# Optimization experiments

Hardware: AMD Instinct MI355X
Metric: run time of the kernel (lower is better)

## Reference

```python
import jax, jax.numpy as jnp
import numpy as np

B, S, D_MODEL, D_HEAD = 8, 2048, 1024, 128
MAX_ROUNDS = 3
THRESH = 0.1
SCALE = 1.0 / np.sqrt(float(D_HEAD))


def setup_inputs() -> dict:
    key = jax.random.key(0)
    ks = jax.random.split(key, 12)

    def lin(k, out_d, in_d):
        # torch Linear weight layout [out, in], y = x @ W.T + b
        return (jax.random.normal(k, (out_d, in_d), jnp.float32) / np.sqrt(float(in_d))).astype(jnp.float32)

    thesis_w = lin(ks[3], D_HEAD, D_HEAD)
    return {
        "x": jax.random.normal(ks[0], (B, S, D_MODEL), jnp.float32),
        "wq": lin(ks[1], D_HEAD, D_MODEL),
        "wk": lin(ks[2], D_HEAD, D_MODEL),
        "wv": lin(ks[4], D_HEAD, D_MODEL),
        "thesis_w": thesis_w,  # antithesis weight is -thesis_w per __init__
        "thesis_b": 0.02 * jax.random.normal(ks[5], (D_HEAD,), jnp.float32),
        "anti_b": 0.02 * jax.random.normal(ks[6], (D_HEAD,), jnp.float32),
        "s_w1": lin(ks[7], D_HEAD, 3 * D_HEAD),
        "s_b1": jnp.zeros((D_HEAD,), jnp.float32),
        "s_w2": lin(ks[8], D_HEAD, D_HEAD),
        "s_b2": jnp.zeros((D_HEAD,), jnp.float32),
        "g_w": lin(ks[9], 1, 2 * D_HEAD),
        "g_b": jnp.zeros((1,), jnp.float32),
    }


def reference(x, wq, wk, wv, thesis_w, thesis_b, anti_b, s_w1, s_b1, s_w2, s_b2, g_w, g_b):
    # q/k/v projections (no bias)
    q = jnp.einsum("bsm,hm->bsh", x, wq)
    k = jnp.einsum("bsm,hm->bsh", x, wk)
    v = jnp.einsum("bsm,hm->bsh", x, wv)

    attn = jax.nn.softmax(jnp.einsum("bqh,bkh->bqk", q, k) * SCALE, axis=-1)
    # dropout is identity at eval time
    cur = jnp.einsum("bqk,bkh->bqh", attn, v)  # [B,S,Dh]

    # attn_weights and v never change across rounds, so thesis/antithesis are
    # round-invariant: compute the context projections once.
    context = cur
    thesis = context @ thesis_w.T + thesis_b
    anti = context @ (-thesis_w).T + anti_b  # antithesis weight = -thesis weight

    active = jnp.ones((B, S), dtype=bool)
    for _ in range(MAX_ROUNDS):
        # emulate `if not active_mask.any(): break` under jit
        any_active = jnp.any(active)
        am = active[..., None].astype(x.dtype)
        at, aa, ac = thesis * am, anti * am, cur * am

        h = jax.nn.relu(jnp.concatenate([at, aa, ac], axis=-1) @ s_w1.T + s_b1)
        synth = h @ s_w2.T + s_b2
        gate = jax.nn.sigmoid(jnp.concatenate([ac, synth], axis=-1) @ g_w.T + g_b)
        update = gate * (synth - ac) * 0.1
        new = cur + update  # applied to ALL tokens, matching original

        stable = jnp.linalg.norm(update, axis=-1) < THRESH  # new - cur == update
        cur = jnp.where(any_active, new, cur)
        active = jnp.where(any_active, active & ~stable, active)
    return cur
```

## Files before the change

kernel.cpp:

```cpp
#include <hip/hip_runtime.h>
#include <hip/hip_bf16.h>

#define B_   8
#define S_   2048
#define DM   1024
#define DH   128
#define BS_  16384
#define SCALE_  0.08838834764831845f
#define SCALE2_ 0.12751744f

typedef unsigned short u16;
typedef unsigned int   u32;
typedef _Float16 half8 __attribute__((ext_vector_type(8)));
typedef __bf16   bf16x8 __attribute__((ext_vector_type(8)));
typedef float    f32x4 __attribute__((ext_vector_type(4)));
typedef u32      u32x4 __attribute__((ext_vector_type(4)));

union H8 { u32x4 v; u32 u[4]; half8 h; bf16x8 b; };

__device__ __forceinline__ float bf2f(u16 u) {
    union { u32 i; float f; } w; w.i = ((u32)u) << 16; return w.f;
}
__device__ __forceinline__ void unpack8(uint4 v, float* f) {
    f[0] = bf2f(v.x & 0xffff); f[1] = bf2f(v.x >> 16);
    f[2] = bf2f(v.y & 0xffff); f[3] = bf2f(v.y >> 16);
    f[4] = bf2f(v.z & 0xffff); f[5] = bf2f(v.z >> 16);
    f[6] = bf2f(v.w & 0xffff); f[7] = bf2f(v.w >> 16);
}
__device__ __forceinline__ float ldE(const void* b, size_t i, int isbf16) {
    return isbf16 ? bf2f(((const u16*)b)[i]) : ((const float*)b)[i];
}
__device__ __forceinline__ void ld8(const void* b, size_t i, int isbf16, float* f) {
    if (isbf16) {
        unpack8(*(const uint4*)((const u16*)b + i), f);
    } else {
        float4 a = *(const float4*)((const float*)b + i);
        float4 c = *(const float4*)((const float*)b + i + 4);
        f[0] = a.x; f[1] = a.y; f[2] = a.z; f[3] = a.w;
        f[4] = c.x; f[5] = c.y; f[6] = c.z; f[7] = c.w;
    }
}
__device__ __forceinline__ u32 f2pk(float v) {
    _Float16 h = (_Float16)v;
    _Float16 l = (_Float16)(v - (float)h);
    union { _Float16 f; u16 u; } a, b; a.f = h; b.f = l;
    return ((u32)a.u << 16) | (u32)b.u;
}
__device__ __forceinline__ void split8(const float* f, u32x4& hi, u32x4& lo) {
    u32 H[8], L[8];
#pragma unroll
    for (int j = 0; j < 8; ++j) {
        _Float16 h = (_Float16)f[j];
        _Float16 l = (_Float16)(f[j] - (float)h);
        union { _Float16 x; u16 u; } a, b; a.x = h; b.x = l;
        H[j] = a.u; L[j] = b.u;
    }
    hi = (u32x4){H[0] | (H[1] << 16), H[2] | (H[3] << 16), H[4] | (H[5] << 16), H[6] | (H[7] << 16)};
    lo = (u32x4){L[0] | (L[1] << 16), L[2] | (L[3] << 16), L[4] | (L[5] << 16), L[6] | (L[7] << 16)};
}
__device__ __forceinline__ u32 permHI(u32 eB, u32 eA) { return __builtin_amdgcn_perm(eB, eA, 0x07060302u); }
__device__ __forceinline__ u16 f2h(float v) { union { _Float16 f; u16 u; } a; a.f = (_Float16)v; return a.u; }
__device__ __forceinline__ float h2f(u16 u) { union { _Float16 f; u16 u; } a; a.u = u; return (float)a.f; }

__global__ void init_kernel(const void* x, int* flag, int* active, int* counts) {
    int i = blockIdx.x * 256 + threadIdx.x;
    if (i < BS_) active[i] = 1;
    if (i < 4) counts[i] = (i == 0) ? BS_ : 0;
    if (i == 0) {
        const u16* w = (const u16*)x;
        int sane = 0;
        for (int t = 0; t < 256; ++t) {
            int e = (w[2 * t] >> 7) & 0xFF;
            if (e >= 100 && e <= 135) ++sane;
        }
        *flag = (sane >= 192) ? 1 : 0;
    }
}

__global__ __launch_bounds__(256) void prepack_w_kernel(
    const void* __restrict__ wq, const void* __restrict__ wk, const void* __restrict__ wv,
    const int* __restrict__ flag, u32x4* __restrict__ wpk)
{
    const int isb = *flag;
    const int gid = blockIdx.x * 256 + threadIdx.x;
    const int l  = gid & 63;
    const int t  = (gid >> 6) & 7;
    const int ks = (gid >> 9) & 31;
    const int z  = gid >> 14;
    const void* W = (z == 0) ? wq : (z == 1) ? wk : wv;
    const int row = 16 * t + (l & 15);
    const int k0  = ks * 32 + 8 * (l >> 4);
    const size_t base = ((((size_t)z * 32 + ks) * 16) + 2 * t) * 64 + l;
    if (isb) {
        uint4 v = *(const uint4*)((const u16*)W + (size_t)row * DM + k0);
        wpk[base] = (u32x4){v.x, v.y, v.z, v.w};
    } else {
        float f[8];
        ld8(W, (size_t)row * DM + k0, 0, f);
        u32x4 hi, lo;
        split8(f, hi, lo);
        wpk[base]      = hi;
        wpk[base + 64] = lo;
    }
}

__global__ __launch_bounds__(256) void qkv_kernel(
    const void* __restrict__ x, const u32x4* __restrict__ wpk,
    const int* __restrict__ flag, u32* __restrict__ qout,
    u32x4* __restrict__ kfrag, u32x4* __restrict__ vfrag)
{
    const int isb = *flag;
    const int z = blockIdx.z;
    const int bx = blockIdx.x;
    const int m0 = ((bx & 7) * 32 + (bx >> 3)) * 64;
    const int tid = threadIdx.x;
    const int wave = tid >> 6, lane = tid & 63;
    const int qd = lane >> 4, c = lane & 15;

    __shared__ u32x4 WLraw[2][16][64];
    u32x4 (*WLb)[2][8][64] = (u32x4(*)[2][8][64])WLraw;
    u32x4 (*WLf)[8][2][64] = (u32x4(*)[8][2][64])WLraw;
    u16 (*TS)[136] = (u16(*)[136])WLraw;

    const u32x4* wz = wpk + (size_t)z * (32 * 16 * 64);
    const size_t arow = (size_t)(m0 + wave * 16 + c) * DM + 8 * qd;

#define STAGE2(i_, b_)                                                            \
    {                                                                             \
        _Pragma("unroll")                                                         \
        for (int _j = 0; _j < 4; ++_j) {                                          \
            const int _g = wave * 4 + _j, _ksub = _g >> 3, _t = _g & 7;           \
            __builtin_amdgcn_global_load_lds(                                     \
                (const __attribute__((address_space(1))) u32*)(                   \
                    wz + ((size_t)(2 * (i_) + _ksub) * 16 + 2 * _t) * 64 + lane), \
                (__attribute__((address_space(3))) u32*)&WLb[b_][_ksub][_t][0],   \
                16, 0, 0);                                                        \
        }                                                                         \
    }
#define STAGE_W(ks_, b_)                                                          \
    {                                                                             \
        const u32x4* _src = wz + ((size_t)(ks_) * 16 + 4 * wave) * 64 + lane;     \
        _Pragma("unroll")                                                         \
        for (int _j = 0; _j < 4; ++_j) {                                          \
            __builtin_amdgcn_global_load_lds(                                     \
                (const __attribute__((address_space(1))) u32*)(_src + _j * 64),   \
                (__attribute__((address_space(3))) u32*)&WLf[b_][2 * wave + (_j >> 1)][_j & 1][0], \
                16, 0, 0);                                                        \
        }                                                                         \
    }

    f32x4 acc[8] = {};

    if (isb) {
        const u16* xb = (const u16*)x;
        uint4 A0 = *(const uint4*)(xb + arow);
        uint4 A1 = *(const uint4*)(xb + arow + 32);
        STAGE2(0, 0);
        uint4 A0n = *(const uint4*)(xb + arow + 64);
        uint4 A1n = *(const uint4*)(xb + arow + 96);
        __syncthreads();
        for (int i = 0; i < 16; ++i) {
            const int cb = i & 1;
            if (i + 1 < 16) STAGE2(i + 1, cb ^ 1);
            H8 Ah0; Ah0.v = (u32x4){A0.x, A0.y, A0.z, A0.w};
            H8 Ah1; Ah1.v = (u32x4){A1.x, A1.y, A1.z, A1.w};
#pragma unroll
            for (int t = 0; t < 8; ++t) {
                H8 bh; bh.v = WLb[cb][0][t][lane];
                acc[t] = __builtin_amdgcn_mfma_f32_16x16x32_bf16(Ah0.b, bh.b, acc[t], 0, 0, 0);
            }
#pragma unroll
            for (int t = 0; t < 8; ++t) {
                H8 bh; bh.v = WLb[cb][1][t][lane];
                acc[t] = __builtin_amdgcn_mfma_f32_16x16x32_bf16(Ah1.b, bh.b, acc[t], 0, 0, 0);
            }
            A0 = A0n; A1 = A1n;
            if (i + 2 < 16) {
                A0n = *(const uint4*)(xb + arow + (size_t)(i + 2) * 64);
                A1n = *(const uint4*)(xb + arow + (size_t)(i + 2) * 64 + 32);
            }
            __syncthreads();
        }
    } else {
        float Ar[8], Arn[8];
        ld8(x, arow, 0, Ar);
        STAGE_W(0, 0);
        ld8(x, arow + 32, 0, Arn);
        __syncthreads();
        for (int ks = 0; ks < 32; ++ks) {
            const int cb = ks & 1;
            if (ks + 1 < 32) STAGE_W(ks + 1, cb ^ 1);
            H8 Ah, Al;
            split8(Ar, Ah.v, Al.v);
#pragma unroll
            for (int t = 0; t < 8; ++t) {
                H8 bh, bl;
                bh.v = WLf[cb][t][0][lane]; bl.v = WLf[cb][t][1][lane];
                acc[t] = __builtin_amdgcn_mfma_f32_16x16x32_f16(Al.h, bh.h, acc[t], 0, 0, 0);
                acc[t] = __builtin_amdgcn_mfma_f32_16x16x32_f16(Ah.h, bl.h, acc[t], 0, 0, 0);
                acc[t] = __builtin_amdgcn_mfma_f32_16x16x32_f16(Ah.h, bh.h, acc[t], 0, 0, 0);
            }
#pragma unroll
            for (int j = 0; j < 8; ++j) Ar[j] = Arn[j];
            if (ks + 2 < 32) ld8(x, arow + (size_t)(ks + 2) * 32, 0, Arn);
            __syncthreads();
        }
    }
#undef STAGE2
#undef STAGE_W

    if (z == 0) {
#pragma unroll
        for (int r = 0; r < 4; ++r) {
            const int row = m0 + wave * 16 + qd * 4 + r;
            u32* op = qout + (size_t)row * DH + c;
#pragma unroll
            for (int t = 0; t < 8; ++t) op[t * 16] = f2pk(acc[t][r]);
        }
    } else {
#pragma unroll
        for (int t = 0; t < 8; ++t)
#pragma unroll
            for (int r = 0; r < 4; ++r)
                TS[wave * 16 + qd * 4 + r][16 * t + c] = f2h(acc[t][r]);
        __syncthreads();
        if (z == 1) {
#pragma unroll
            for (int i = 0; i < 4; ++i) {
                const int f = tid + 256 * i;
                const int lf = f & 63, ks = (f >> 6) & 3, sub = f >> 8;
                const int key = sub * 16 + (lf & 15);
                const int d0  = ks * 32 + 8 * (lf >> 4);
                u32 w[4];
#pragma unroll
                for (int q = 0; q < 4; ++q)
                    w[q] = (u32)TS[key][d0 + 2 * q] | ((u32)TS[key][d0 + 2 * q + 1] << 16);
                kfrag[((size_t)(m0 / 16 + sub) * 4 + ks) * 64 + lf] = (u32x4){w[0], w[1], w[2], w[3]};
            }
        } else {
#pragma unroll
            for (int i = 0; i < 4; ++i) {
                const int f = tid + 256 * i;
                const int lf = f & 63, t = (f >> 6) & 7, sub = f >> 9;
                const int kb2 = sub * 32 + 8 * (lf >> 4);
                const int dh  = 16 * t + (lf & 15);
                u32 w[4];
#pragma unroll
                for (int q = 0; q < 4; ++q)
                    w[q] = (u32)TS[kb2 + 2 * q][dh] | ((u32)TS[kb2 + 2 * q + 1][dh] << 16);
                vfrag[((size_t)(m0 / 32 + sub) * 8 + t) * 64 + lf] = (u32x4){w[0], w[1], w[2], w[3]};
            }
        }
    }
}

template <bool WRITE_PARTIAL>
__device__ __forceinline__ void attn_body(
    const u32* qp, const u32x4* __restrict__ kfrag, const u32x4* __restrict__ vfrag,
    u16* outO, u16* outL, float* cur,
    int b, int q0, int kt0, int kt1, int part)
{
    const int tid = threadIdx.x;
    const int wave = tid >> 6, lane = tid & 63;
    const int qd = lane >> 4, c = lane & 15;

    __shared__ __align__(16) u16 PB[4][640];

    H8 Qh[4];
    {
        const u32* qr = qp + ((size_t)b * S_ + q0 + wave * 16 + c) * DH;
#pragma unroll
        for (int ks = 0; ks < 4; ++ks) {
            uint4 e0 = *(const uint4*)(qr + ks * 32 + qd * 8);
            uint4 e1 = *(const uint4*)(qr + ks * 32 + qd * 8 + 4);
            Qh[ks].u[0] = permHI(e0.y, e0.x); Qh[ks].u[1] = permHI(e0.w, e0.z);
            Qh[ks].u[2] = permHI(e1.y, e1.x); Qh[ks].u[3] = permHI(e1.w, e1.z);
        }
    }

    f32x4 O[8] = {};
    float lsum[4] = {};

    const u32x4* kb0 = kfrag + (size_t)b * 128 * 256;
    const u32x4* vb0 = vfrag + (size_t)b * 64 * 512;

    for (int kt = kt0; kt < kt1; ++kt) {
        const u32x4* kf = kb0 + (size_t)kt * 512;
        const u32x4* vf = vb0 + (size_t)kt * 512;

        f32x4 S0 = {}, S1 = {};
        __builtin_amdgcn_s_setprio(1);
#pragma unroll
        for (int ks = 0; ks < 4; ++ks) {
            H8 kh;
            kh.v = kf[ks * 64 + lane];
            S0 = __builtin_amdgcn_mfma_f32_16x16x32_f16(Qh[ks].h, kh.h, S0, 0, 0, 0);
            kh.v = kf[256 + ks * 64 + lane];
            S1 = __builtin_amdgcn_mfma_f32_16x16x32_f16(Qh[ks].h, kh.h, S1, 0, 0, 0);
        }
        __builtin_amdgcn_s_setprio(0);

        u16* pw = PB[wave];
#pragma unroll
        for (int r = 0; r < 4; ++r) {
            float e0 = exp2f(fmaf(S0[r], SCALE2_, -4.0f));
            float e1 = exp2f(fmaf(S1[r], SCALE2_, -4.0f));
            lsum[r] += e0 + e1;
            pw[(4 * qd + r) * 40 + c]      = f2h(e0);
            pw[(4 * qd + r) * 40 + 16 + c] = f2h(e1);
        }

        uint4 ev = *(const uint4*)&pw[c * 40 + 8 * qd];
        H8 Ph;
        Ph.u[0] = ev.x; Ph.u[1] = ev.y; Ph.u[2] = ev.z; Ph.u[3] = ev.w;

        __builtin_amdgcn_s_setprio(1);
#pragma unroll
        for (int t = 0; t < 8; ++t) {
            H8 vh;
            vh.v = vf[t * 64 + lane];
            O[t] = __builtin_amdgcn_mfma_f32_16x16x32_f16(Ph.h, vh.h, O[t], 0, 0, 0);
        }
        __builtin_amdgcn_s_setprio(0);
    }

    if (WRITE_PARTIAL) {
        float lred[4];
#pragma unroll
        for (int r = 0; r < 4; ++r) {
            float l = lsum[r];
            l += __shfl_xor(l, 1); l += __shfl_xor(l, 2);
            l += __shfl_xor(l, 4); l += __shfl_xor(l, 8);
            lred[r] = l;
        }
        const size_t rb = (size_t)b * S_ + q0 + wave * 16 + 4 * qd;
        u16* Op = outO + (size_t)part * ((size_t)BS_ * DH);
#pragma unroll
        for (int t = 0; t < 8; ++t)
#pragma unroll
            for (int r = 0; r < 4; ++r)
                Op[(rb + r) * DH + t * 16 + c] = f2h(O[t][r]);
        if (c == 0) {
            u16* lp = outL + (size_t)part * BS_;
#pragma unroll
            for (int r = 0; r < 4; ++r) lp[rb + r] = f2h(lred[r]);
        }
    } else {
        float linv[4];
#pragma unroll
        for (int r = 0; r < 4; ++r) {
            float l = lsum[r];
            l += __shfl_xor(l, 1); l += __shfl_xor(l, 2);
            l += __shfl_xor(l, 4); l += __shfl_xor(l, 8);
            linv[r] = 1.0f / l;
        }
        const size_t rb = (size_t)b * S_ + q0 + wave * 16 + 4 * qd;
#pragma unroll
        for (int t = 0; t < 8; ++t)
#pragma unroll
            for (int r = 0; r < 4; ++r)
                cur[(rb + r) * DH + t * 16 + c] = O[t][r] * linv[r];
    }
}

__global__ __launch_bounds__(256) void attn_kernel(
    const u32* qp, const u32x4* __restrict__ kfrag, const u32x4* __restrict__ vfrag, float* cur)
{
    const int rid = blockIdx.x + 32 * blockIdx.y;
    attn_body<false>(qp, kfrag, vfrag, nullptr, nullptr, cur,
                     rid & 7, ((rid >> 3) & 31) * 64, 0, S_ / 32, 0);
}

__global__ __launch_bounds__(256) void attn_split_kernel(
    const u32* qp, const u32x4* __restrict__ kfrag, const u32x4* __restrict__ vfrag,
    u16* __restrict__ Opart, u16* __restrict__ lpart)
{
    const int rid = blockIdx.x + 32 * (blockIdx.y + 8 * blockIdx.z);
    const int b    = rid & 7;
    const int qx   = (rid >> 3) & 31;
    const int part = rid >> 8;
    const int quart = S_ / 128;
    attn_body<true>(qp, kfrag, vfrag, Opart, lpart, nullptr,
                    b, qx * 64, part * quart, (part + 1) * quart, part);
}

__global__ __launch_bounds__(256) void combine_kernel(
    const u16* __restrict__ Opart, const u16* __restrict__ lpart,
    float* __restrict__ cur)
{
    const size_t N1 = (size_t)BS_ * DH;
    const size_t i0 = ((size_t)blockIdx.x * 256 + threadIdx.x) * 16;
    const int row = (int)(i0 >> 7);
    const float lt = h2f(lpart[row]) + h2f(lpart[BS_ + row])
                   + h2f(lpart[2 * BS_ + row]) + h2f(lpart[3 * BS_ + row]);
    const float linv = 1.0f / lt;
    float acc[16] = {};
#pragma unroll
    for (int p = 0; p < 4; ++p) {
        const u16* op = Opart + (size_t)p * N1 + i0;
        uint4 v0 = *(const uint4*)op;
        uint4 v1 = *(const uint4*)(op + 8);
        const u32 w[8] = {v0.x, v0.y, v0.z, v0.w, v1.x, v1.y, v1.z, v1.w};
#pragma unroll
        for (int j = 0; j < 8; ++j) {
            acc[2 * j]     += h2f((u16)(w[j] & 0xffff));
            acc[2 * j + 1] += h2f((u16)(w[j] >> 16));
        }
    }
#pragma unroll
    for (int t = 0; t < 4; ++t)
        *(float4*)(cur + i0 + t * 4) = make_float4(
            acc[4*t] * linv, acc[4*t+1] * linv, acc[4*t+2] * linv, acc[4*t+3] * linv);
}

__global__ __launch_bounds__(256) void prepack_rw_kernel(
    const void* __restrict__ tw, const void* __restrict__ w1, const void* __restrict__ w2,
    const int* __restrict__ flag, u32x4* __restrict__ pk)
{
    const int isb = *flag;
    const int gid = blockIdx.x * 256 + threadIdx.x;
    const int l = gid & 63, t = (gid >> 6) & 7, ks = (gid >> 9) & 3, mat = gid >> 11;
    const int row = 16 * t + (l & 15);
    const int k0  = ks * 32 + 8 * (l >> 4);
    float f[8];
    if (mat == 0)      ld8(tw, (size_t)row * DH + k0, isb, f);
    else if (mat <= 3) ld8(w1, (size_t)row * 384 + (mat - 1) * 128 + k0, isb, f);
    else               ld8(w2, (size_t)row * DH + k0, isb, f);
    u32x4 hi, lo;
    split8(f, hi, lo);
    const size_t base = (((size_t)mat * 4 + ks) * 16 + 2 * t) * 64 + l;
    pk[base] = hi; pk[base + 64] = lo;
}

struct Afrag { H8 h[4], l[4]; };
__device__ __forceinline__ void splitA(const float (&A)[4][8], Afrag& F) {
#pragma unroll
    for (int ks = 0; ks < 4; ++ks) split8(A[ks], F.h[ks].v, F.l[ks].v);
}

__global__ __launch_bounds__(256) void round_kernel(
    const float* cur0, const float* curr,
    const u32x4* __restrict__ pk, u16* __restrict__ T0,
    const void* __restrict__ tb, const void* __restrict__ ab,
    const void* __restrict__ b1, const void* __restrict__ b2,
    const void* __restrict__ gw, const void* __restrict__ gb,
    const int* __restrict__ flag, int* active, int* counts, int r,
    float* cur_out, void* dout)
{
    const int isb = *flag;
    const int tok0 = blockIdx.x * 32;
    const int tid = threadIdx.x;
    const bool last = (dout != nullptr);

    if (counts[r] <= 0) {
        if (last) {
            for (int e = tid; e < 32 * DH; e += 256) {
                size_t idx = (size_t)tok0 * DH + e;
                float v = curr[idx];
                if (isb) ((__hip_bfloat16*)dout)[idx] = __float2bfloat16(v);
                else     ((float*)dout)[idx] = v;
            }
        }
        return;
    }

    const int wave = tid >> 6, lane = tid & 63;
    const int qd = lane >> 4, c = lane & 15;
    const int rowg = wave >> 1, colh = wave & 1;

    __shared__ u32x4 WB[2][4][8][64];
    __shared__ u16 TS[32][132];
    __shared__ float actS[32], tbS[128], abS[128], b1S[128], b2S[128], gwS[256];
    __shared__ int blkcnt;

    auto stageB = [&](int mat, int buf) {
#pragma unroll
        for (int j = 0; j < 8; ++j) {
            const int g = wave * 8 + j, ks = g >> 3, t = g & 7;
            __builtin_amdgcn_global_load_lds(
                (const __attribute__((address_space(1))) u32*)(
                    pk + (((size_t)mat * 4 + ks) * 16 + 2 * t) * 64 + lane),
                (__attribute__((address_space(3))) u32*)&WB[buf][ks][t][0],
                16, 0, 0);
        }
    };
    auto stageF = [&](int mat, int h, int buf) {
#pragma unroll
        for (int j = 0; j < 8; ++j) {
            const int g = wave * 8 + j, kl = g >> 4, p = (g >> 3) & 1, t = g & 7;
            __builtin_amdgcn_global_load_lds(
                (const __attribute__((address_space(1))) u32*)(
                    pk + (((size_t)mat * 4 + 2 * h + kl) * 16 + 2 * t + p) * 64 + lane),
                (__attribute__((address_space(3))) u32*)&WB[buf][kl * 2 + p][t][0],
                16, 0, 0);
        }
    };
    auto gemmB = [&](const Afrag& F, int buf, f32x4 (&acc)[4]) {
#pragma unroll
        for (int ks = 0; ks < 4; ++ks)
#pragma unroll
            for (int tl = 0; tl < 4; ++tl) {
                H8 bh; bh.v = WB[buf][ks][4 * colh + tl][lane];
                acc[tl] = __builtin_amdgcn_mfma_f32_16x16x32_f16(F.l[ks].h, bh.h, acc[tl], 0, 0, 0);
                acc[tl] = __builtin_amdgcn_mfma_f32_16x16x32_f16(F.h[ks].h, bh.h, acc[tl], 0, 0, 0);
            }
    };
    auto gemmFh = [&](const Afrag& F, int h, int buf, f32x4 (&acc)[4]) {
#pragma unroll
        for (int kl = 0; kl < 2; ++kl) {
            const int ks = 2 * h + kl;
#pragma unroll
            for (int tl = 0; tl < 4; ++tl) {
                H8 bh, bl;
                bh.v = WB[buf][kl * 2][4 * colh + tl][lane];
                bl.v = WB[buf][kl * 2 + 1][4 * colh + tl][lane];
                acc[tl] = __builtin_amdgcn_mfma_f32_16x16x32_f16(F.l[ks].h, bh.h, acc[tl], 0, 0, 0);
                acc[tl] = __builtin_amdgcn_mfma_f32_16x16x32_f16(F.h[ks].h, bl.h, acc[tl], 0, 0, 0);
                acc[tl] = __builtin_amdgcn_mfma_f32_16x16x32_f16(F.h[ks].h, bh.h, acc[tl], 0, 0, 0);
            }
        }
    };
    auto STAGE = [&](int mat, int buf) { if (isb) stageB(mat, buf); else stageF(mat, 0, buf); };
    auto GEMM = [&](int mat, const Afrag& F, int buf, f32x4 (&acc)[4]) {
        if (isb) {
            gemmB(F, buf, acc);
        } else {
            gemmFh(F, 0, buf, acc);
            __syncthreads();
            stageF(mat, 1, buf);
            __syncthreads();
            gemmFh(F, 1, buf, acc);
        }
    };

    if (r == 0) STAGE(0, 0); else STAGE(1, 1);
    if (tid < 32) actS[tid] = active[tok0 + tid] ? 1.0f : 0.0f;
    if (tid < 128) {
        tbS[tid] = ldE(tb, tid, isb); abS[tid] = ldE(ab, tid, isb);
        b1S[tid] = ldE(b1, tid, isb); b2S[tid] = ldE(b2, tid, isb);
    }
    gwS[tid] = ldE(gw, tid, isb);
    if (tid == 0) blkcnt = 0;
    const float gbf = ldE(gb, 0, isb);

    const int rowl = 16 * rowg + c;
    const int hr   = 16 * rowg + 4 * qd;

    Afrag FA;
    if (r == 0) {
        float A1[4][8];
        const float* cr = cur0 + (size_t)(tok0 + rowl) * DH;
#pragma unroll
        for (int ks = 0; ks < 4; ++ks) {
            *(float4*)&A1[ks][0] = *(const float4*)(cr + ks * 32 + 8 * qd);
            *(float4*)&A1[ks][4] = *(const float4*)(cr + ks * 32 + 8 * qd + 4);
        }
        splitA(A1, FA);
    } else {
        for (int i = tid; i < 32 * 64; i += 256) {
            const int row = i >> 6, c2 = (i & 63) * 2;
            *(u32*)&TS[row][c2] = *(const u32*)&T0[(size_t)(tok0 + row) * DH + c2];
        }
    }
    __syncthreads();

    if (r == 0) {
        STAGE(1, 1);
        f32x4 accT[4] = {};
        GEMM(0, FA, 0, accT);
#pragma unroll
        for (int tl = 0; tl < 4; ++tl)
#pragma unroll
            for (int rr = 0; rr < 4; ++rr)
                TS[hr + rr][16 * (4 * colh + tl) + c] = f2h(accT[tl][rr]);
        __syncthreads();
        for (int i = tid; i < 32 * 64; i += 256) {
            const int row = i >> 6, c2 = (i & 63) * 2;
            *(u32*)&T0[(size_t)(tok0 + row) * DH + c2] = *(const u32*)&TS[row][c2];
        }
    }

    STAGE(2, 0);
    f32x4 acc1[4] = {};
    const float am_r = actS[rowl];
    {
        float Ac[4][8];
#pragma unroll
        for (int ks = 0; ks < 4; ++ks)
#pragma unroll
            for (int j = 0; j < 8; ++j) {
                const int k = ks * 32 + 8 * qd + j;
                Ac[ks][j] = (h2f(TS[rowl][k]) + tbS[k]) * am_r;
            }
        Afrag FC; splitA(Ac, FC);
        GEMM(1, FC, 1, acc1);
    }
    __syncthreads();

    STAGE(3, 1);
    {
        float Ac[4][8];
#pragma unroll
        for (int ks = 0; ks < 4; ++ks)
#pragma unroll
            for (int j = 0; j < 8; ++j) {
                const int k = ks * 32 + 8 * qd + j;
                Ac[ks][j] = (abS[k] - h2f(TS[rowl][k])) * am_r;
            }
        Afrag FC; splitA(Ac, FC);
        GEMM(2, FC, 0, acc1);
    }
    __syncthreads();

    STAGE(4, 0);
    {
        float Ac[4][8];
        const float* cr = curr + (size_t)(tok0 + rowl) * DH;
#pragma unroll
        for (int ks = 0; ks < 4; ++ks) {
            float4 a0 = *(const float4*)(cr + ks * 32 + 8 * qd);
            float4 a1 = *(const float4*)(cr + ks * 32 + 8 * qd + 4);
            Ac[ks][0] = a0.x * am_r; Ac[ks][1] = a0.y * am_r;
            Ac[ks][2] = a0.z * am_r; Ac[ks][3] = a0.w * am_r;
            Ac[ks][4] = a1.x * am_r; Ac[ks][5] = a1.y * am_r;
            Ac[ks][6] = a1.z * am_r; Ac[ks][7] = a1.w * am_r;
        }
        Afrag FC; splitA(Ac, FC);
        GEMM(3, FC, 1, acc1);
    }
#pragma unroll
    for (int tl = 0; tl < 4; ++tl)
#pragma unroll
        for (int rr = 0; rr < 4; ++rr) {
            const int col = 16 * (4 * colh + tl) + c;
            TS[hr + rr][col] = f2h(fmaxf(acc1[tl][rr] + b1S[col], 0.0f));
        }
    __syncthreads();

    {
        float Ac[4][8];
#pragma unroll
        for (int ks = 0; ks < 4; ++ks)
#pragma unroll
            for (int j = 0; j < 8; ++j)
                Ac[ks][j] = h2f(TS[rowl][ks * 32 + 8 * qd + j]);
        Afrag FC; splitA(Ac, FC);
        f32x4 acc2[4] = {};
        GEMM(4, FC, 0, acc2);
        __syncthreads();
#pragma unroll
        for (int tl = 0; tl < 4; ++tl)
#pragma unroll
            for (int rr = 0; rr < 4; ++rr) {
                const int col = 16 * (4 * colh + tl) + c;
                TS[hr + rr][col] = f2h(acc2[tl][rr] + b2S[col]);
            }
    }
    __syncthreads();

    const int tok = tid >> 3, d0 = (tid & 7) * 16;
    const float am = actS[tok];
    const float* cp = curr + (size_t)(tok0 + tok) * DH + d0;
    float cv[16];
#pragma unroll
    for (int t = 0; t < 4; ++t) {
        float4 vv = *(const float4*)(cp + t * 4);
        cv[t * 4] = vv.x; cv[t * 4 + 1] = vv.y; cv[t * 4 + 2] = vv.z; cv[t * 4 + 3] = vv.w;
    }
    float srow[16];
#pragma unroll
    for (int e = 0; e < 16; ++e) srow[e] = h2f(TS[tok][d0 + e]);
    float gp = 0.0f;
#pragma unroll
    for (int e = 0; e < 16; ++e)
        gp += cv[e] * am * gwS[d0 + e] + srow[e] * gwS[128 + d0 + e];
    gp += __shfl_xor(gp, 1, 8);
    gp += __shfl_xor(gp, 2, 8);
    gp += __shfl_xor(gp, 4, 8);
    const float gate = 1.0f / (1.0f + __expf(-(gp + gbf)));
    float ss = 0.0f; float up[16];
#pragma unroll
    for (int e = 0; e < 16; ++e) {
        float u = gate * (srow[e] - cv[e] * am) * 0.1f;
        up[e] = u; ss += u * u;
    }
    ss += __shfl_xor(ss, 1, 8);
    ss += __shfl_xor(ss, 2, 8);
    ss += __shfl_xor(ss, 4, 8);
    const bool stable = sqrtf(ss) < 0.1f;

    if (last) {
        size_t off = (size_t)(tok0 + tok) * DH + d0;
        if (isb) {
            __hip_bfloat16* op = (__hip_bfloat16*)dout + off;
#pragma unroll
            for (int e = 0; e < 16; ++e) op[e] = __float2bfloat16(cv[e] + up[e]);
        } else {
            float* op = (float*)dout + off;
#pragma unroll
            for (int t = 0; t < 4; ++t)
                *(float4*)(op + t * 4) = make_float4(cv[t * 4] + up[t * 4], cv[t * 4 + 1] + up[t * 4 + 1],
                                                     cv[t * 4 + 2] + up[t * 4 + 2], cv[t * 4 + 3] + up[t * 4 + 3]);
        }
    } else {
        float* op = cur_out + (size_t)(tok0 + tok) * DH + d0;
#pragma unroll
        for (int t = 0; t < 4; ++t)
            *(float4*)(op + t * 4) = make_float4(cv[t * 4] + up[t * 4], cv[t * 4 + 1] + up[t * 4 + 1],
                                                 cv[t * 4 + 2] + up[t * 4 + 2], cv[t * 4 + 3] + up[t * 4 + 3]);
    }
    const int newact = (am > 0.0f && !stable) ? 1 : 0;
    if ((tid & 7) == 0) {
        active[tok0 + tok] = newact;
        if (newact) atomicAdd(&blkcnt, 1);
    }
    __syncthreads();
    if (tid == 0 && blkcnt > 0) atomicAdd(&counts[r + 1], blkcnt);
}

extern "C" void kernel_launch(void* const* d_in, const int* in_sizes, int n_in,
                              void* d_out, int out_size, void* d_ws, size_t ws_size,
                              hipStream_t stream) {
    const void* x  = d_in[0];
    const void* wq = d_in[1];
    const void* wk = d_in[2];
    const void* wv = d_in[3];
    const void* tw = d_in[4];
    const void* tb = d_in[5];
    const void* ab = d_in[6];
    const void* w1 = d_in[7];
    const void* b1 = d_in[8];
    const void* w2 = d_in[9];
    const void* b2 = d_in[10];
    const void* gw = d_in[11];
    const void* gb = d_in[12];

    u32* ws = (u32*)d_ws;
    const size_t N1 = (size_t)BS_ * DH;
    u32* qp = ws;
    u32* kp = ws + N1;
    u32* vp = ws + 2 * N1;
    int* active = (int*)(ws + 3 * N1);
    int* counts = active + BS_;
    int* flag   = counts + 4;
    float* cur0  = (float*)qp;
    float* cur_r = (float*)kp;
    u16* Opart16 = (u16*)(ws + 3 * N1 + 32768);
    u16* lpart16 = (u16*)(ws + 5 * N1 + 32768);
    const bool big_ws = ws_size >= (size_t)42300000;
    u32x4* wpk = (u32x4*)(ws + 3 * N1 + 32768);
    u32x4* pkRW = (u32x4*)vp;
    u16*   T0c  = (u16*)(vp + 131072);
    u32x4* kfragP = (u32x4*)kp;
    u32x4* vfragP = (u32x4*)vp;

    init_kernel<<<dim3(BS_ / 256), 256, 0, stream>>>(x, flag, active, counts);
    prepack_w_kernel<<<dim3(192), 256, 0, stream>>>(wq, wk, wv, flag, wpk);
    qkv_kernel<<<dim3(BS_ / 64, 1, 3), 256, 0, stream>>>(x, wpk, flag, qp, kfragP, vfragP);
    if (big_ws) {
        attn_split_kernel<<<dim3(S_ / 64, B_, 4), 256, 0, stream>>>(qp, kfragP, vfragP, Opart16, lpart16);
        combine_kernel<<<dim3(512), 256, 0, stream>>>(Opart16, lpart16, cur0);
    } else {
        attn_kernel<<<dim3(S_ / 64, B_), 256, 0, stream>>>(qp, kfragP, vfragP, cur0);
    }
    prepack_rw_kernel<<<dim3(40), 256, 0, stream>>>(tw, w1, w2, flag, pkRW);
    round_kernel<<<dim3(BS_ / 32), 256, 0, stream>>>(
        cur0, cur0, pkRW, T0c, tb, ab, b1, b2, gw, gb, flag, active, counts, 0, cur_r, nullptr);
    round_kernel<<<dim3(BS_ / 32), 256, 0, stream>>>(
        cur0, cur_r, pkRW, T0c, tb, ab, b1, b2, gw, gb, flag, active, counts, 1, cur_r, nullptr);
    round_kernel<<<dim3(BS_ / 32), 256, 0, stream>>>(
        cur0, cur_r, pkRW, T0c, tb, ab, b1, b2, gw, gb, flag, active, counts, 2, cur_r, d_out);
}
```

Baseline: 254.7 us.

## Halve round-kernel token tile to 16 and stream weights in half-K stages

The round kernel now handles 16 tokens per block instead of 32, doubling the grid to 1024 blocks. Each wave owns two output column tiles across all 16 rows. Weight staging is split into half-K (bf16) or quarter-K (fp32) chunks in a smaller double-buffered LDS area, which lets the next chunk load while the current one is multiplied. This is meant to raise parallelism and occupancy for the small per-round GEMMs, at the cost of loading each weight matrix twice as often per token and adding more barriers.

```diff
diff --git a/kernel.cpp b/kernel.cpp
--- a/kernel.cpp
+++ b/kernel.cpp
@@ -448,13 +448,13 @@
     float* cur_out, void* dout)
 {
     const int isb = *flag;
-    const int tok0 = blockIdx.x * 32;
+    const int tok0 = blockIdx.x * 16;
     const int tid = threadIdx.x;
     const bool last = (dout != nullptr);
 
     if (counts[r] <= 0) {
         if (last) {
-            for (int e = tid; e < 32 * DH; e += 256) {
+            for (int e = tid; e < 16 * DH; e += 256) {
                 size_t idx = (size_t)tok0 * DH + e;
                 float v = curr[idx];
                 if (isb) ((__hip_bfloat16*)dout)[idx] = __float2bfloat16(v);
@@ -466,124 +466,80 @@
 
     const int wave = tid >> 6, lane = tid & 63;
     const int qd = lane >> 4, c = lane & 15;
-    const int rowg = wave >> 1, colh = wave & 1;
-
-    __shared__ u32x4 WB[2][4][8][64];
-    __shared__ u16 TS[32][132];
-    __shared__ float actS[32], tbS[128], abS[128], b1S[128], b2S[128], gwS[256];
+
+    __shared__ u32x4 WB[2][2][8][64];
+    __shared__ u16 TS[16][132];
+    __shared__ float actS[16], tbS[128], abS[128], b1S[128], b2S[128], gwS[256];
     __shared__ int blkcnt;
 
-    auto stageB = [&](int mat, int buf) {
-#pragma unroll
-        for (int j = 0; j < 8; ++j) {
-            const int g = wave * 8 + j, ks = g >> 3, t = g & 7;
+    auto stageBh = [&](int mat, int h) {
+#pragma unroll
+        for (int j = 0; j < 4; ++j) {
+            const int g = wave * 4 + j, kl = g >> 3, t = g & 7;
             __builtin_amdgcn_global_load_lds(
                 (const __attribute__((address_space(1))) u32*)(
-                    pk + (((size_t)mat * 4 + ks) * 16 + 2 * t) * 64 + lane),
-                (__attribute__((address_space(3))) u32*)&WB[buf][ks][t][0],
+                    pk + (((size_t)mat * 4 + 2 * h + kl) * 16 + 2 * t) * 64 + lane),
+                (__attribute__((address_space(3))) u32*)&WB[h][kl][t][0],
                 16, 0, 0);
         }
     };
-    auto stageF = [&](int mat, int h, int buf) {
-#pragma unroll
-        for (int j = 0; j < 8; ++j) {
-            const int g = wave * 8 + j, kl = g >> 4, p = (g >> 3) & 1, t = g & 7;
+    auto gemmBh = [&](const Afrag& F, int h, f32x4 (&acc)[2]) {
+#pragma unroll
+        for (int kl = 0; kl < 2; ++kl) {
+            const int ks = 2 * h + kl;
+#pragma unroll
+            for (int tl = 0; tl < 2; ++tl) {
+                H8 bh; bh.v = WB[h][kl][2 * wave + tl][lane];
+                acc[tl] = __builtin_amdgcn_mfma_f32_16x16x32_f16(F.l[ks].h, bh.h, acc[tl], 0, 0, 0);
+                acc[tl] = __builtin_amdgcn_mfma_f32_16x16x32_f16(F.h[ks].h, bh.h, acc[tl], 0, 0, 0);
+            }
+        }
+    };
+    auto stageFq = [&](int mat, int q, int buf) {
+#pragma unroll
+        for (int j = 0; j < 4; ++j) {
+            const int g = wave * 4 + j, p = g & 1, t = g >> 1;
             __builtin_amdgcn_global_load_lds(
                 (const __attribute__((address_space(1))) u32*)(
-                    pk + (((size_t)mat * 4 + 2 * h + kl) * 16 + 2 * t + p) * 64 + lane),
-                (__attribute__((address_space(3))) u32*)&WB[buf][kl * 2 + p][t][0],
+                    pk + (((size_t)mat * 4 + q) * 16 + 2 * t + p) * 64 + lane),
+                (__attribute__((address_space(3))) u32*)&WB[buf][p][t][0],
                 16, 0, 0);
         }
     };
-    auto gemmB = [&](const Afrag& F, int buf, f32x4 (&acc)[4]) {
-#pragma unroll
-        for (int ks = 0; ks < 4; ++ks)
-#pragma unroll
-            for (int tl = 0; tl < 4; ++tl) {
-                H8 bh; bh.v = WB[buf][ks][4 * colh + tl][lane];
-                acc[tl] = __builtin_amdgcn_mfma_f32_16x16x32_f16(F.l[ks].h, bh.h, acc[tl], 0, 0, 0);
-                acc[tl] = __builtin_amdgcn_mfma_f32_16x16x32_f16(F.h[ks].h, bh.h, acc[tl], 0, 0, 0);
-            }
-    };
-    auto gemmFh = [&](const Afrag& F, int h, int buf, f32x4 (&acc)[4]) {
-#pragma unroll
-        for (int kl = 0; kl < 2; ++kl) {
-            const int ks = 2 * h + kl;
-#pragma unroll
-            for (int tl = 0; tl < 4; ++tl) {
-                H8 bh, bl;
-                bh.v = WB[buf][kl * 2][4 * colh + tl][lane];
-                bl.v = WB[buf][kl * 2 + 1][4 * colh + tl][lane];
-                acc[tl] = __builtin_amdgcn_mfma_f32_16x16x32_f16(F.l[ks].h, bh.h, acc[tl], 0, 0, 0);
-                acc[tl] = __builtin_amdgcn_mfma_f32_16x16x32_f16(F.h[ks].h, bl.h, acc[tl], 0, 0, 0);
-                acc[tl] = __builtin_amdgcn_mfma_f32_16x16x32_f16(F.h[ks].h, bh.h, acc[tl], 0, 0, 0);
-            }
-        }
-    };
-    auto STAGE = [&](int mat, int buf) { if (isb) stageB(mat, buf); else stageF(mat, 0, buf); };
-    auto GEMM = [&](int mat, const Afrag& F, int buf, f32x4 (&acc)[4]) {
-        if (isb) {
-            gemmB(F, buf, acc);
-        } else {
-            gemmFh(F, 0, buf, acc);
-            __syncthreads();
-            stageF(mat, 1, buf);
-            __syncthreads();
-            gemmFh(F, 1, buf, acc);
-        }
-    };
-
-    if (r == 0) STAGE(0, 0); else STAGE(1, 1);
-    if (tid < 32) actS[tid] = active[tok0 + tid] ? 1.0f : 0.0f;
-    if (tid < 128) {
-        tbS[tid] = ldE(tb, tid, isb); abS[tid] = ldE(ab, tid, isb);
-        b1S[tid] = ldE(b1, tid, isb); b2S[tid] = ldE(b2, tid, isb);
-    }
-    gwS[tid] = ldE(gw, tid, isb);
-    if (tid == 0) blkcnt = 0;
-    const float gbf = ldE(gb, 0, isb);
-
-    const int rowl = 16 * rowg + c;
-    const int hr   = 16 * rowg + 4 * qd;
-
-    Afrag FA;
-    if (r == 0) {
-        float A1[4][8];
-        const float* cr = cur0 + (size_t)(tok0 + rowl) * DH;
-#pragma unroll
-        for (int ks = 0; ks < 4; ++ks) {
-            *(float4*)&A1[ks][0] = *(const float4*)(cr + ks * 32 + 8 * qd);
-            *(float4*)&A1[ks][4] = *(const float4*)(cr + ks * 32 + 8 * qd + 4);
-        }
-        splitA(A1, FA);
-    } else {
-        for (int i = tid; i < 32 * 64; i += 256) {
-            const int row = i >> 6, c2 = (i & 63) * 2;
-            *(u32*)&TS[row][c2] = *(const u32*)&T0[(size_t)(tok0 + row) * DH + c2];
-        }
-    }
-    __syncthreads();
-
-    if (r == 0) {
-        STAGE(1, 1);
-        f32x4 accT[4] = {};
-        GEMM(0, FA, 0, accT);
-#pragma unroll
-        for (int tl = 0; tl < 4; ++tl)
-#pragma unroll
-            for (int rr = 0; rr < 4; ++rr)
-                TS[hr + rr][16 * (4 * colh + tl) + c] = f2h(accT[tl][rr]);
-        __syncthreads();
-        for (int i = tid; i < 32 * 64; i += 256) {
-            const int row = i >> 6, c2 = (i & 63) * 2;
-            *(u32*)&T0[(size_t)(tok0 + row) * DH + c2] = *(const u32*)&TS[row][c2];
-        }
-    }
-
-    STAGE(2, 0);
-    f32x4 acc1[4] = {};
-    const float am_r = actS[rowl];
-    {
+    auto gemmFq = [&](const Afrag& F, int q, int buf, f32x4 (&acc)[2]) {
+#pragma unroll
+        for (int tl = 0; tl < 2; ++tl) {
+            H8 bh, bl;
+            bh.v = WB[buf][0][2 * wave + tl][lane];
+            bl.v = WB[buf][1][2 * wave + tl][lane];
+            acc[tl] = __builtin_amdgcn_mfma_f32_16x16x32_f16(F.l[q].h, bh.h, acc[tl], 0, 0, 0);
+            acc[tl] = __builtin_amdgcn_mfma_f32_16x16x32_f16(F.h[q].h, bl.h, acc[tl], 0, 0, 0);
+            acc[tl] = __builtin_amdgcn_mfma_f32_16x16x32_f16(F.h[q].h, bh.h, acc[tl], 0, 0, 0);
+        }
+    };
+    auto GEMMF = [&](int mat, const Afrag& F, f32x4 (&acc)[2]) {
+        for (int q = 0; q < 4; ++q) {
+            stageFq(mat, q, q & 1);
+            __syncthreads();
+            gemmFq(F, q, q & 1, acc);
+            __syncthreads();
+        }
+    };
+
+    const int hr = 4 * qd;
+    const int rowl = c;
+
+    auto writeTS = [&](const f32x4 (&acc)[2], const float* bias, bool relu) {
+#pragma unroll
+        for (int tl = 0; tl < 2; ++tl)
+#pragma unroll
+            for (int rr = 0; rr < 4; ++rr) {
+                const int col = 16 * (2 * wave + tl) + c;
+                float v = acc[tl][rr] + (bias ? bias[col] : 0.0f);
+                TS[hr + rr][col] = f2h(relu ? fmaxf(v, 0.0f) : v);
+            }
+    };
+    auto buildAt = [&](Afrag& F, float am_r) {
         float Ac[4][8];
 #pragma unroll
         for (int ks = 0; ks < 4; ++ks)
@@ -592,13 +548,9 @@
                 const int k = ks * 32 + 8 * qd + j;
                 Ac[ks][j] = (h2f(TS[rowl][k]) + tbS[k]) * am_r;
             }
-        Afrag FC; splitA(Ac, FC);
-        GEMM(1, FC, 1, acc1);
-    }
-    __syncthreads();
-
-    STAGE(3, 1);
-    {
+        splitA(Ac, F);
+    };
+    auto buildAa = [&](Afrag& F, float am_r) {
         float Ac[4][8];
 #pragma unroll
         for (int ks = 0; ks < 4; ++ks)
@@ -607,13 +559,9 @@
                 const int k = ks * 32 + 8 * qd + j;
                 Ac[ks][j] = (abS[k] - h2f(TS[rowl][k])) * am_r;
             }
-        Afrag FC; splitA(Ac, FC);
-        GEMM(2, FC, 0, acc1);
-    }
-    __syncthreads();
-
-    STAGE(4, 0);
-    {
+        splitA(Ac, F);
+    };
+    auto buildAc = [&](Afrag& F, float am_r) {
         float Ac[4][8];
         const float* cr = curr + (size_t)(tok0 + rowl) * DH;
 #pragma unroll
@@ -625,68 +573,173 @@
             Ac[ks][4] = a1.x * am_r; Ac[ks][5] = a1.y * am_r;
             Ac[ks][6] = a1.z * am_r; Ac[ks][7] = a1.w * am_r;
         }
-        Afrag FC; splitA(Ac, FC);
-        GEMM(3, FC, 1, acc1);
-    }
-#pragma unroll
-    for (int tl = 0; tl < 4; ++tl)
-#pragma unroll
-        for (int rr = 0; rr < 4; ++rr) {
-            const int col = 16 * (4 * colh + tl) + c;
-            TS[hr + rr][col] = f2h(fmaxf(acc1[tl][rr] + b1S[col], 0.0f));
-        }
-    __syncthreads();
-
-    {
+        splitA(Ac, F);
+    };
+    auto buildAh = [&](Afrag& F) {
         float Ac[4][8];
 #pragma unroll
         for (int ks = 0; ks < 4; ++ks)
 #pragma unroll
             for (int j = 0; j < 8; ++j)
                 Ac[ks][j] = h2f(TS[rowl][ks * 32 + 8 * qd + j]);
-        Afrag FC; splitA(Ac, FC);
-        f32x4 acc2[4] = {};
-        GEMM(4, FC, 0, acc2);
+        splitA(Ac, F);
+    };
+
+    if (tid < 16) actS[tid] = active[tok0 + tid] ? 1.0f : 0.0f;
+    if (tid < 128) {
+        tbS[tid] = ldE(tb, tid, isb); abS[tid] = ldE(ab, tid, isb);
+        b1S[tid] = ldE(b1, tid, isb); b2S[tid] = ldE(b2, tid, isb);
+    }
+    gwS[tid] = ldE(gw, tid, isb);
+    if (tid == 0) blkcnt = 0;
+    const float gbf = ldE(gb, 0, isb);
+
+    if (isb) {
+        f32x4 acc1[2] = {};
+        if (r == 0) {
+            float A1[4][8];
+            const float* cr = cur0 + (size_t)(tok0 + rowl) * DH;
+#pragma unroll
+            for (int ks = 0; ks < 4; ++ks) {
+                *(float4*)&A1[ks][0] = *(const float4*)(cr + ks * 32 + 8 * qd);
+                *(float4*)&A1[ks][4] = *(const float4*)(cr + ks * 32 + 8 * qd + 4);
+            }
+            Afrag FA; splitA(A1, FA);
+            stageBh(0, 0);
+            __syncthreads();
+            stageBh(0, 1);
+            f32x4 accT[2] = {};
+            gemmBh(FA, 0, accT);
+            __syncthreads();
+            stageBh(1, 0);
+            gemmBh(FA, 1, accT);
+            writeTS(accT, nullptr, false);
+            __syncthreads();
+            for (int i = tid; i < 16 * 64; i += 256) {
+                const int row = i >> 6, c2 = (i & 63) * 2;
+                *(u32*)&T0[(size_t)(tok0 + row) * DH + c2] = *(const u32*)&TS[row][c2];
+            }
+        } else {
+            stageBh(1, 0);
+            for (int i = tid; i < 16 * 64; i += 256) {
+                const int row = i >> 6, c2 = (i & 63) * 2;
+                *(u32*)&TS[row][c2] = *(const u32*)&T0[(size_t)(tok0 + row) * DH + c2];
+            }
+            __syncthreads();
+        }
+        const float am_r = actS[rowl];
+        {
+            Afrag FC; buildAt(FC, am_r);
+            stageBh(1, 1);
+            gemmBh(FC, 0, acc1);
+            __syncthreads();
+            stageBh(2, 0);
+            gemmBh(FC, 1, acc1);
+            __syncthreads();
+        }
+        {
+            Afrag FC; buildAa(FC, am_r);
+            stageBh(2, 1);
+            gemmBh(FC, 0, acc1);
+            __syncthreads();
+            stageBh(3, 0);
+            gemmBh(FC, 1, acc1);
+            __syncthreads();
+        }
+        {
+            Afrag FC; buildAc(FC, am_r);
+            stageBh(3, 1);
+            gemmBh(FC, 0, acc1);
+            __syncthreads();
+            stageBh(4, 0);
+            gemmBh(FC, 1, acc1);
+        }
+        writeTS(acc1, b1S, true);
         __syncthreads();
-#pragma unroll
-        for (int tl = 0; tl < 4; ++tl)
-#pragma unroll
-            for (int rr = 0; rr < 4; ++rr) {
-                const int col = 16 * (4 * colh + tl) + c;
-                TS[hr + rr][col] = f2h(acc2[tl][rr] + b2S[col]);
-            }
-    }
-    __syncthreads();
-
-    const int tok = tid >> 3, d0 = (tid & 7) * 16;
+        {
+            Afrag FC; buildAh(FC);
+            stageBh(4, 1);
+            f32x4 acc2[2] = {};
+            gemmBh(FC, 0, acc2);
+            __syncthreads();
+            gemmBh(FC, 1, acc2);
+            writeTS(acc2, b2S, false);
+        }
+        __syncthreads();
+    } else {
+        __syncthreads();
+        f32x4 acc1[2] = {};
+        if (r == 0) {
+            float A1[4][8];
+            const float* cr = cur0 + (size_t)(tok0 + rowl) * DH;
+#pragma unroll
+            for (int ks = 0; ks < 4; ++ks) {
+                *(float4*)&A1[ks][0] = *(const float4*)(cr + ks * 32 + 8 * qd);
+                *(float4*)&A1[ks][4] = *(const float4*)(cr + ks * 32 + 8 * qd + 4);
+            }
+            Afrag FA; splitA(A1, FA);
+            f32x4 accT[2] = {};
+            GEMMF(0, FA, accT);
+            writeTS(accT, nullptr, false);
+            __syncthreads();
+            for (int i = tid; i < 16 * 64; i += 256) {
+                const int row = i >> 6, c2 = (i & 63) * 2;
+                *(u32*)&T0[(size_t)(tok0 + row) * DH + c2] = *(const u32*)&TS[row][c2];
+            }
+        } else {
+            for (int i = tid; i < 16 * 64; i += 256) {
+                const int row = i >> 6, c2 = (i & 63) * 2;
+                *(u32*)&TS[row][c2] = *(const u32*)&T0[(size_t)(tok0 + row) * DH + c2];
+            }
+            __syncthreads();
+        }
+        const float am_r = actS[rowl];
+        { Afrag FC; buildAt(FC, am_r); GEMMF(1, FC, acc1); }
+        { Afrag FC; buildAa(FC, am_r); GEMMF(2, FC, acc1); }
+        { Afrag FC; buildAc(FC, am_r); GEMMF(3, FC, acc1); }
+        writeTS(acc1, b1S, true);
+        __syncthreads();
+        {
+            Afrag FC; buildAh(FC);
+            f32x4 acc2[2] = {};
+            GEMMF(4, FC, acc2);
+            writeTS(acc2, b2S, false);
+        }
+        __syncthreads();
+    }
+
+    const int tok = tid >> 4, d0 = (tid & 15) * 8;
     const float am = actS[tok];
     const float* cp = curr + (size_t)(tok0 + tok) * DH + d0;
-    float cv[16];
-#pragma unroll
-    for (int t = 0; t < 4; ++t) {
-        float4 vv = *(const float4*)(cp + t * 4);
-        cv[t * 4] = vv.x; cv[t * 4 + 1] = vv.y; cv[t * 4 + 2] = vv.z; cv[t * 4 + 3] = vv.w;
-    }
-    float srow[16];
-#pragma unroll
-    for (int e = 0; e < 16; ++e) srow[e] = h2f(TS[tok][d0 + e]);
+    float cv[8];
+    {
+        float4 v0 = *(const float4*)cp;
+        float4 v1 = *(const float4*)(cp + 4);
+        cv[0] = v0.x; cv[1] = v0.y; cv[2] = v0.z; cv[3] = v0.w;
+        cv[4] = v1.x; cv[5] = v1.y; cv[6] = v1.z; cv[7] = v1.w;
+    }
+    float srow[8];
+#pragma unroll
+    for (int e = 0; e < 8; ++e) srow[e] = h2f(TS[tok][d0 + e]);
     float gp = 0.0f;
 #pragma unroll
-    for (int e = 0; e < 16; ++e)
+    for (int e = 0; e < 8; ++e)
         gp += cv[e] * am * gwS[d0 + e] + srow[e] * gwS[128 + d0 + e];
-    gp += __shfl_xor(gp, 1, 8);
-    gp += __shfl_xor(gp, 2, 8);
-    gp += __shfl_xor(gp, 4, 8);
+    gp += __shfl_xor(gp, 1, 16);
+    gp += __shfl_xor(gp, 2, 16);
+    gp += __shfl_xor(gp, 4, 16);
+    gp += __shfl_xor(gp, 8, 16);
     const float gate = 1.0f / (1.0f + __expf(-(gp + gbf)));
-    float ss = 0.0f; float up[16];
-#pragma unroll
-    for (int e = 0; e < 16; ++e) {
+    float ss = 0.0f; float up[8];
+#pragma unroll
+    for (int e = 0; e < 8; ++e) {
         float u = gate * (srow[e] - cv[e] * am) * 0.1f;
         up[e] = u; ss += u * u;
     }
-    ss += __shfl_xor(ss, 1, 8);
-    ss += __shfl_xor(ss, 2, 8);
-    ss += __shfl_xor(ss, 4, 8);
+    ss += __shfl_xor(ss, 1, 16);
+    ss += __shfl_xor(ss, 2, 16);
+    ss += __shfl_xor(ss, 4, 16);
+    ss += __shfl_xor(ss, 8, 16);
     const bool stable = sqrtf(ss) < 0.1f;
 
     if (last) {
@@ -694,23 +747,19 @@
         if (isb) {
             __hip_bfloat16* op = (__hip_bfloat16*)dout + off;
 #pragma unroll
-            for (int e = 0; e < 16; ++e) op[e] = __float2bfloat16(cv[e] + up[e]);
+            for (int e = 0; e < 8; ++e) op[e] = __float2bfloat16(cv[e] + up[e]);
         } else {
             float* op = (float*)dout + off;
-#pragma unroll
-            for (int t = 0; t < 4; ++t)
-                *(float4*)(op + t * 4) = make_float4(cv[t * 4] + up[t * 4], cv[t * 4 + 1] + up[t * 4 + 1],
-                                                     cv[t * 4 + 2] + up[t * 4 + 2], cv[t * 4 + 3] + up[t * 4 + 3]);
+            *(float4*)op       = make_float4(cv[0] + up[0], cv[1] + up[1], cv[2] + up[2], cv[3] + up[3]);
+            *(float4*)(op + 4) = make_float4(cv[4] + up[4], cv[5] + up[5], cv[6] + up[6], cv[7] + up[7]);
         }
     } else {
         float* op = cur_out + (size_t)(tok0 + tok) * DH + d0;
-#pragma unroll
-        for (int t = 0; t < 4; ++t)
-            *(float4*)(op + t * 4) = make_float4(cv[t * 4] + up[t * 4], cv[t * 4 + 1] + up[t * 4 + 1],
-                                                 cv[t * 4 + 2] + up[t * 4 + 2], cv[t * 4 + 3] + up[t * 4 + 3]);
+        *(float4*)op       = make_float4(cv[0] + up[0], cv[1] + up[1], cv[2] + up[2], cv[3] + up[3]);
+        *(float4*)(op + 4) = make_float4(cv[4] + up[4], cv[5] + up[5], cv[6] + up[6], cv[7] + up[7]);
     }
     const int newact = (am > 0.0f && !stable) ? 1 : 0;
-    if ((tid & 7) == 0) {
+    if ((tid & 15) == 0) {
         active[tok0 + tok] = newact;
         if (newact) atomicAdd(&blkcnt, 1);
     }
@@ -764,10 +813,10 @@
         attn_kernel<<<dim3(S_ / 64, B_), 256, 0, stream>>>(qp, kfragP, vfragP, cur0);
     }
     prepack_rw_kernel<<<dim3(40), 256, 0, stream>>>(tw, w1, w2, flag, pkRW);
-    round_kernel<<<dim3(BS_ / 32), 256, 0, stream>>>(
+    round_kernel<<<dim3(BS_ / 16), 256, 0, stream>>>(
         cur0, cur0, pkRW, T0c, tb, ab, b1, b2, gw, gb, flag, active, counts, 0, cur_r, nullptr);
-    round_kernel<<<dim3(BS_ / 32), 256, 0, stream>>>(
+    round_kernel<<<dim3(BS_ / 16), 256, 0, stream>>>(
         cur0, cur_r, pkRW, T0c, tb, ab, b1, b2, gw, gb, flag, active, counts, 1, cur_r, nullptr);
-    round_kernel<<<dim3(BS_ / 32), 256, 0, stream>>>(
+    round_kernel<<<dim3(BS_ / 16), 256, 0, stream>>>(
         cur0, cur_r, pkRW, T0c, tb, ab, b1, b2, gw, gb, flag, active, counts, 2, cur_r, d_out);
 }
```

Measured after the change: 255.9 us. Within noise of the previous version (+0.5%).
